# Performance work log

Measured on AMD Instinct MI355X. Metric: run time of the kernel, lower is better.

## Reference

```python
import jax, jax.numpy as jnp
import numpy as np

LN_EPS = 1e-5
MASK_FILL = -1e10


def setup_inputs() -> dict:
    key = jax.random.key(0)
    ks = jax.random.split(key, 6)
    b, lq, lk, d = 8, 2048, 2048, 256
    q = jax.random.normal(ks[0], (b, lq, d), dtype=jnp.float32)
    k = jax.random.normal(ks[1], (b, lk, d), dtype=jnp.float32)
    v = jax.random.normal(ks[2], (b, lk, d), dtype=jnp.float32)
    # additive-score weight, scaled so logits are O(1)
    shared_attn = jax.random.normal(ks[3], (1, 2 * d), dtype=jnp.float32) / jnp.sqrt(jnp.float32(2 * d))
    fc_w = jax.random.normal(ks[4], (d, d), dtype=jnp.float32) / jnp.sqrt(jnp.float32(d))
    ln_gamma = jnp.ones((d,), dtype=jnp.float32)
    ln_beta = jnp.zeros((d,), dtype=jnp.float32)
    mask = jax.random.randint(ks[5], (b, lq, lk), 0, 2).astype(bool)
    return {"q": q, "k": k, "v": v, "shared_attn": shared_attn,
            "fc_w": fc_w, "ln_gamma": ln_gamma, "ln_beta": ln_beta, "mask": mask}


def reference(q, k, v, shared_attn, fc_w, ln_gamma, ln_beta, mask):
    d_k = q.shape[-1]
    residual = q
    # F.linear(cat([q_exp, k_exp], -1), W) with W:(1, 2*d_k) decomposes as
    # score[b,i,j] = q[b,i] . w_q + k[b,j] . w_k  (rank-1 additive score)
    w_q = shared_attn[0, :d_k]
    w_k = shared_attn[0, d_k:]
    sq = jnp.einsum('bid,d->bi', q, w_q)          # (b, lq)
    sk = jnp.einsum('bjd,d->bj', k, w_k)          # (b, lk)
    attn = sq[:, :, None] + sk[:, None, :]        # (b, lq, lk)
    attn = jnp.where(mask, jnp.float32(MASK_FILL), attn)
    attn = jax.nn.softmax(attn, axis=2)
    out = jnp.einsum('bij,bjd->bid', attn, v)     # (b, lq, d_v)
    out = out @ fc_w.T                            # F.linear(out, fc_w)
    x = out + residual
    mu = jnp.mean(x, axis=-1, keepdims=True)
    var = jnp.var(x, axis=-1, keepdims=True)
    out = (x - mu) / jnp.sqrt(var + LN_EPS) * ln_gamma + ln_beta
    return (out, attn)
```

## Files before the change

### kernel.cpp

```cpp
#include <hip/hip_runtime.h>
#include <hip/hip_bf16.h>

#define BB 8
#define LQ 2048
#define LK 2048
#define DD 256
#define OUT0_N (BB*LQ*DD)

typedef short s16x8 __attribute__((ext_vector_type(8)));
typedef float f32x4 __attribute__((ext_vector_type(4)));

__device__ __forceinline__ unsigned short f2b(float x){
  unsigned int u = __float_as_uint(x);
  u += 0x7fffu + ((u >> 16) & 1u);
  return (unsigned short)(u >> 16);
}
__device__ __forceinline__ float b2f(unsigned short h){
  return __uint_as_float(((unsigned int)h) << 16);
}
__device__ __forceinline__ float ldf(const void* p, long i, int bf){
  return bf ? b2f(((const unsigned short*)p)[i]) : ((const float*)p)[i];
}
__device__ __forceinline__ s16x8 ld8(const void* p, long i, int bf){
  if (bf) return *(const s16x8*)((const unsigned short*)p + i);
  const float* f = (const float*)p + i;
  float4 a = *(const float4*)(f);
  float4 c = *(const float4*)(f + 4);
  s16x8 r;
  r[0]=(short)f2b(a.x); r[1]=(short)f2b(a.y); r[2]=(short)f2b(a.z); r[3]=(short)f2b(a.w);
  r[4]=(short)f2b(c.x); r[5]=(short)f2b(c.y); r[6]=(short)f2b(c.z); r[7]=(short)f2b(c.w);
  return r;
}
__device__ __forceinline__ float wsum(float v){
  #pragma unroll
  for (int o=32;o;o>>=1) v += __shfl_xor(v, o, 64);
  return v;
}

__device__ __forceinline__ void detect_flags(const void* q, const void* mask,
                                             int& mbytes, int& bf){
  __shared__ int s_bf, s_mb;
  int t = threadIdx.x;
  if (t == 0){ s_bf = 0; s_mb = 0; }
  __syncthreads();
  if (t < 256){
    float x = fabsf(((const float*)q)[t]);
    if (x > 1e-6f && x < 100.0f) atomicAdd(&s_bf, 1);
    unsigned int mw = ((const unsigned int*)mask)[t];
    if (mw > 1u) atomicOr(&s_mb, 1);
  }
  __syncthreads();
  bf = (s_bf < 128) ? 1 : 0;
  mbytes = s_mb;
}

__global__ __launch_bounds__(256) void k_prep(const void* q, const void* kk,
    const void* v, const void* sh, const void* fc, const void* mask,
    float* e, unsigned short* vtf){
  int mbytes, bf;
  detect_flags(q, mask, mbytes, bf);
  (void)mbytes;
  int lane = threadIdx.x & 63;

  if (blockIdx.x >= 1024){
    int wid = ((blockIdx.x - 1024) << 2) + (threadIdx.x >> 6);
    long base = (long)wid * DD + lane * 4;
    float acc;
    if (bf){
      ushort4 kv = *(const ushort4*)((const unsigned short*)kk + base);
      ushort4 wv = *(const ushort4*)((const unsigned short*)sh + DD + lane*4);
      acc = b2f(kv.x)*b2f(wv.x) + b2f(kv.y)*b2f(wv.y)
          + b2f(kv.z)*b2f(wv.z) + b2f(kv.w)*b2f(wv.w);
    } else {
      float4 kv = *(const float4*)((const float*)kk + base);
      float4 wv = *(const float4*)((const float*)sh + DD + lane*4);
      acc = kv.x*wv.x + kv.y*wv.y + kv.z*wv.z + kv.w*wv.w;
    }
    acc = wsum(acc);
    if (lane == 0) e[wid] = __expf(acc);
    return;
  }

  int wid  = (blockIdx.x << 2) + (threadIdx.x >> 6);
  int dbase = (wid & 15) << 4;
  int jbase = (wid >> 4) << 6;
  int r = lane & 15, g = lane >> 4;
  f32x4 acc[4];
  #pragma unroll
  for (int t2=0;t2<4;t2++) acc[t2] = (f32x4){0.f,0.f,0.f,0.f};
  #pragma unroll
  for (int ks = 0; ks < 8; ++ks){
    int k0 = ks*32 + g*8;
    s16x8 bv = ld8(fc, (long)(dbase + r)*DD + k0, bf);
    #pragma unroll
    for (int t2 = 0; t2 < 4; ++t2){
      s16x8 a = ld8(v, (long)(jbase + t2*16 + r)*DD + k0, bf);
      acc[t2] = __builtin_amdgcn_mfma_f32_16x16x32_bf16(a, bv, acc[t2], 0, 0, 0);
    }
  }
  int b  = jbase >> 11;
  int jj = jbase & 2047;
  int d  = dbase + r;
  #pragma unroll
  for (int t2 = 0; t2 < 4; ++t2){
    int kidx = (jj >> 3) + t2*2 + (g >> 1);
    long idx = ((long)(b*256 + kidx))*2048 + (long)d*8 + (g & 1)*4;
    ushort4 w4;
    w4.x = f2b(acc[t2][0]); w4.y = f2b(acc[t2][1]);
    w4.z = f2b(acc[t2][2]); w4.w = f2b(acc[t2][3]);
    *(ushort4*)(vtf + idx) = w4;
  }
}

__device__ __forceinline__ s16x8 afrag(const unsigned int (*bits_s)[66],
    const unsigned short* e16_s, int row, int kk){
  int w0 = (kk >> 2) & 63;
  int nib4 = (kk >> 8) << 2;
  unsigned lo = (bits_s[row][w0]   >> nib4) & 0xFu;
  unsigned hi = (bits_s[row][w0+1] >> nib4) & 0xFu;
  unsigned m8 = lo | (hi << 4);
  union { s16x8 v; unsigned u[4]; } a;
  a.v = *(const s16x8*)(&e16_s[kk]);
  #pragma unroll
  for (int i = 0; i < 4; ++i){
    unsigned w = a.u[i];
    w = (m8 & (1u << (2*i)))   ? (w & 0xFFFF0000u) : w;
    w = (m8 & (1u << (2*i+1))) ? (w & 0x0000FFFFu) : w;
    a.u[i] = w;
  }
  return a.v;
}

__global__ __launch_bounds__(512, 4) void k_pvf(void* d_out, const unsigned short* vtf,
    const void* q, const void* gamp, const void* betp, const void* mask,
    const float* e){
  __shared__ unsigned int bits_s[32][66];
  __shared__ __align__(16) unsigned short e16_s[LK];
  __shared__ __align__(16) float red[2][32][132];
  __shared__ float scale_s[32];
  __shared__ float gs[256], bs[256];
  int mbytes, bf;
  detect_flags(q, mask, mbytes, bf);
  int o     = ((blockIdx.x & 7) << 6) + (blockIdx.x >> 3);
  int b     = o >> 6;
  int rbase = (o & 63) << 5;
  int t = threadIdx.x, lane = t & 63, wid = t >> 6;
  int nh = wid & 1, ks = wid >> 1;
  int r16 = lane >> 4, c16 = lane & 15;
  int dbase = nh << 7;
  const float* eb = e + b * LK;

  { float4 ef = ((const float4*)eb)[t];
    ushort4 u; u.x=f2b(ef.x); u.y=f2b(ef.y); u.z=f2b(ef.z); u.w=f2b(ef.w);
    *(ushort4*)(&e16_s[t*4]) = u; }
  if (t < 256){ gs[t] = ldf(gamp, t, bf); bs[t] = ldf(betp, t, bf); }

  unsigned short* attn16 = (unsigned short*)d_out + OUT0_N;
  float*          attn32 = (float*)d_out + OUT0_N;
  #pragma unroll 1
  for (int rr = 0; rr < 4; ++rr){
    int row = (wid << 2) + rr;
    long rowm = ((long)(b*LQ + rbase + row)) * (long)LK;
    unsigned int bw = 0;
    float4 ev[8];
    float s = 0.f;
    #pragma unroll
    for (int w = 0; w < 8; ++w){
      int j = (w << 8) + (lane << 2);
      unsigned int m4;
      if (mbytes){
        unsigned int mb = *(const unsigned int*)((const unsigned char*)mask + rowm + j);
        m4 = (mb & 1u) | ((mb >> 7) & 2u) | ((mb >> 14) & 4u) | ((mb >> 21) & 8u);
      } else {
        int4 mi = *(const int4*)((const int*)mask + rowm + j);
        m4 = (mi.x?1u:0u) | (mi.y?2u:0u) | (mi.z?4u:0u) | (mi.w?8u:0u);
      }
      bw |= m4 << (w*4);
      ev[w] = *(const float4*)(eb + j);
      if (!(m4 & 1u)) s += ev[w].x;
      if (!(m4 & 2u)) s += ev[w].y;
      if (!(m4 & 4u)) s += ev[w].z;
      if (!(m4 & 8u)) s += ev[w].w;
    }
    s = wsum(s);
    float scal = (s > 0.f) ? (1.0f/s) : -1.0f;
    bits_s[row][lane] = bw;
    if (lane == 0) scale_s[row] = scal;
    #pragma unroll
    for (int w = 0; w < 8; ++w){
      int j = (w << 8) + (lane << 2);
      float p0,p1,p2,p3;
      if (scal < 0.f){ p0=p1=p2=p3 = 1.0f/2048.0f; }
      else {
        p0 = (bw >> (w*4  )) & 1u ? 0.f : ev[w].x * scal;
        p1 = (bw >> (w*4+1)) & 1u ? 0.f : ev[w].y * scal;
        p2 = (bw >> (w*4+2)) & 1u ? 0.f : ev[w].z * scal;
        p3 = (bw >> (w*4+3)) & 1u ? 0.f : ev[w].w * scal;
      }
      if (bf){
        ushort4 u4; u4.x=f2b(p0); u4.y=f2b(p1); u4.z=f2b(p2); u4.w=f2b(p3);
        *(ushort4*)(attn16 + rowm + j) = u4;
      } else {
        float4 f4 = {p0,p1,p2,p3};
        *(float4*)(attn32 + rowm + j) = f4;
      }
    }
  }
  __syncthreads();

  float sc0 = scale_s[c16];
  float sc1 = scale_s[16 + c16];
  s16x8 cf;
  #pragma unroll
  for (int i = 0; i < 8; ++i) cf[i] = (short)0x3A00;

  const unsigned short* vtfb = vtf + (long)b * 256 * 2048;
  f32x4 acc[2][8];
  #pragma unroll
  for (int i=0;i<2;i++)
    #pragma unroll
    for (int j=0;j<8;j++) acc[i][j] = (f32x4){0.f,0.f,0.f,0.f};

  for (int s = 0; s < 16; ++s){
    int k0 = (ks << 9) + (s << 5);
    const unsigned short* bp = vtfb + ((long)((k0 >> 3) + r16)*256 + dbase + c16)*8;
    s16x8 A0 = (sc0 < 0.f) ? cf : afrag(bits_s, e16_s, c16,      k0 + r16*8);
    s16x8 A1 = (sc1 < 0.f) ? cf : afrag(bits_s, e16_s, 16 + c16, k0 + r16*8);
    {
      s16x8 B0 = *(const s16x8*)(bp);
      s16x8 B1 = *(const s16x8*)(bp + 128);
      s16x8 B2 = *(const s16x8*)(bp + 256);
      s16x8 B3 = *(const s16x8*)(bp + 384);
      acc[0][0] = __builtin_amdgcn_mfma_f32_16x16x32_bf16(A0, B0, acc[0][0], 0,0,0);
      acc[1][0] = __builtin_amdgcn_mfma_f32_16x16x32_bf16(A1, B0, acc[1][0], 0,0,0);
      acc[0][1] = __builtin_amdgcn_mfma_f32_16x16x32_bf16(A0, B1, acc[0][1], 0,0,0);
      acc[1][1] = __builtin_amdgcn_mfma_f32_16x16x32_bf16(A1, B1, acc[1][1], 0,0,0);
      acc[0][2] = __builtin_amdgcn_mfma_f32_16x16x32_bf16(A0, B2, acc[0][2], 0,0,0);
      acc[1][2] = __builtin_amdgcn_mfma_f32_16x16x32_bf16(A1, B2, acc[1][2], 0,0,0);
      acc[0][3] = __builtin_amdgcn_mfma_f32_16x16x32_bf16(A0, B3, acc[0][3], 0,0,0);
      acc[1][3] = __builtin_amdgcn_mfma_f32_16x16x32_bf16(A1, B3, acc[1][3], 0,0,0);
    }
    {
      s16x8 B4 = *(const s16x8*)(bp + 512);
      s16x8 B5 = *(const s16x8*)(bp + 640);
      s16x8 B6 = *(const s16x8*)(bp + 768);
      s16x8 B7 = *(const s16x8*)(bp + 896);
      acc[0][4] = __builtin_amdgcn_mfma_f32_16x16x32_bf16(A0, B4, acc[0][4], 0,0,0);
      acc[1][4] = __builtin_amdgcn_mfma_f32_16x16x32_bf16(A1, B4, acc[1][4], 0,0,0);
      acc[0][5] = __builtin_amdgcn_mfma_f32_16x16x32_bf16(A0, B5, acc[0][5], 0,0,0);
      acc[1][5] = __builtin_amdgcn_mfma_f32_16x16x32_bf16(A1, B5, acc[1][5], 0,0,0);
      acc[0][6] = __builtin_amdgcn_mfma_f32_16x16x32_bf16(A0, B6, acc[0][6], 0,0,0);
      acc[1][6] = __builtin_amdgcn_mfma_f32_16x16x32_bf16(A1, B6, acc[1][6], 0,0,0);
      acc[0][7] = __builtin_amdgcn_mfma_f32_16x16x32_bf16(A0, B7, acc[0][7], 0,0,0);
      acc[1][7] = __builtin_amdgcn_mfma_f32_16x16x32_bf16(A1, B7, acc[1][7], 0,0,0);
    }
  }

  #pragma unroll
  for (int r = 1; r < 4; ++r){
    if (ks == r){
      #pragma unroll
      for (int mi = 0; mi < 2; ++mi)
        #pragma unroll
        for (int ni = 0; ni < 8; ++ni)
          #pragma unroll
          for (int reg = 0; reg < 4; ++reg)
            red[nh][mi*16 + r16*4 + reg][ni*16 + c16] = acc[mi][ni][reg];
    }
    __syncthreads();
    if (ks == 0){
      #pragma unroll
      for (int mi = 0; mi < 2; ++mi)
        #pragma unroll
        for (int ni = 0; ni < 8; ++ni)
          #pragma unroll
          for (int reg = 0; reg < 4; ++reg)
            acc[mi][ni][reg] += red[nh][mi*16 + r16*4 + reg][ni*16 + c16];
    }
    __syncthreads();
  }
  if (ks == 0){
    #pragma unroll
    for (int mi = 0; mi < 2; ++mi)
      #pragma unroll
      for (int ni = 0; ni < 8; ++ni)
        #pragma unroll
        for (int reg = 0; reg < 4; ++reg)
          red[nh][mi*16 + r16*4 + reg][ni*16 + c16] = acc[mi][ni][reg];
  }
  __syncthreads();

  {
    int row = t >> 4, cg = t & 15;
    int nh2 = cg >> 3, coff = (cg & 7) << 4;
    float sc = scale_s[row];
    float sce = (sc < 0.f) ? 1.0f : sc;
    long grow = (long)b*LQ + rbase + row;
    float xv[16];
    float ps = 0.f, pq = 0.f;
    #pragma unroll
    for (int i4 = 0; i4 < 4; ++i4){
      float4 rv = *(const float4*)(&red[nh2][row][coff + i4*4]);
      float rr[4] = {rv.x, rv.y, rv.z, rv.w};
      int col0 = (cg << 4) + i4*4;
      float qv[4];
      if (bf){
        ushort4 qu = *(const ushort4*)((const unsigned short*)q + grow*DD + col0);
        qv[0]=b2f(qu.x); qv[1]=b2f(qu.y); qv[2]=b2f(qu.z); qv[3]=b2f(qu.w);
      } else {
        float4 qf = *(const float4*)((const float*)q + grow*DD + col0);
        qv[0]=qf.x; qv[1]=qf.y; qv[2]=qf.z; qv[3]=qf.w;
      }
      #pragma unroll
      for (int i = 0; i < 4; ++i){
        float x = rr[i]*sce + qv[i];
        xv[i4*4 + i] = x;
        ps += x; pq += x*x;
      }
    }
    ps += __shfl_xor(ps, 1, 64); pq += __shfl_xor(pq, 1, 64);
    ps += __shfl_xor(ps, 2, 64); pq += __shfl_xor(pq, 2, 64);
    ps += __shfl_xor(ps, 4, 64); pq += __shfl_xor(pq, 4, 64);
    ps += __shfl_xor(ps, 8, 64); pq += __shfl_xor(pq, 8, 64);
    float mu = ps * (1.0f/256.0f);
    float var = pq * (1.0f/256.0f) - mu*mu;
    float rs = rsqrtf(var + 1e-5f);
    #pragma unroll
    for (int i4 = 0; i4 < 4; ++i4){
      int col0 = (cg << 4) + i4*4;
      float y[4];
      #pragma unroll
      for (int i = 0; i < 4; ++i){
        int col = col0 + i;
        y[i] = (xv[i4*4 + i] - mu) * rs * gs[col] + bs[col];
      }
      long oi = grow*(long)DD + col0;
      if (bf){
        ushort4 u4; u4.x=f2b(y[0]); u4.y=f2b(y[1]); u4.z=f2b(y[2]); u4.w=f2b(y[3]);
        *(ushort4*)((unsigned short*)d_out + oi) = u4;
      } else {
        float4 f4 = {y[0],y[1],y[2],y[3]};
        *(float4*)((float*)d_out + oi) = f4;
      }
    }
  }
}

extern "C" void kernel_launch(void* const* d_in, const int* in_sizes, int n_in,
                              void* d_out, int out_size, void* d_ws, size_t ws_size,
                              hipStream_t stream) {
  const void* q    = d_in[0];
  const void* k    = d_in[1];
  const void* v    = d_in[2];
  const void* sh   = d_in[3];
  const void* fc   = d_in[4];
  const void* gam  = d_in[5];
  const void* bet  = d_in[6];
  const void* mask = d_in[7];

  float*          e   = (float*)((char*)d_ws + 65536);
  unsigned short* vtf = (unsigned short*)((char*)d_ws + 4456448);

  k_prep<<<5120, 256, 0, stream>>>(q, k, v, sh, fc, mask, e, vtf);
  k_pvf <<<512,  512, 0, stream>>>(d_out, vtf, q, gam, bet, mask, e);
}
```

Baseline: 130.3 us.

## Stream V tiles into LDS with async global_load_lds double buffering

Replaces the direct global-to-register loads of V fragments in the PV MFMA loop with per-wave double-buffered asynchronous global_load_lds transfers, gated by explicit vmcnt waits and sched barriers. The reduction buffer is aliased onto the same shared memory region so the staging space fits. The goal is to overlap V fetch latency with MFMA work. The risk is that the larger LDS footprint (about 80KB per block) lowers occupancy, and the manual waitcnt and barrier scheduling constrains the compiler.

```diff
diff --git a/kernel.cpp b/kernel.cpp
--- a/kernel.cpp
+++ b/kernel.cpp
@@ -9,6 +9,9 @@
 
 typedef short s16x8 __attribute__((ext_vector_type(8)));
 typedef float f32x4 __attribute__((ext_vector_type(4)));
+
+#define GAS __attribute__((address_space(1)))
+#define LAS __attribute__((address_space(3)))
 
 __device__ __forceinline__ unsigned short f2b(float x){
   unsigned int u = __float_as_uint(x);
@@ -134,11 +137,15 @@
 __global__ __launch_bounds__(512, 4) void k_pvf(void* d_out, const unsigned short* vtf,
     const void* q, const void* gamp, const void* betp, const void* mask,
     const float* e){
-  __shared__ unsigned int bits_s[32][66];
-  __shared__ __align__(16) unsigned short e16_s[LK];
-  __shared__ __align__(16) float red[2][32][132];
-  __shared__ float scale_s[32];
-  __shared__ float gs[256], bs[256];
+  __shared__ __align__(16) char smem[80256];
+  unsigned int (*bits_s)[66] = reinterpret_cast<unsigned int(*)[66]>(smem + 65536);
+  unsigned short* e16_s      = (unsigned short*)(smem + 73984);
+  float* scale_s             = (float*)(smem + 78080);
+  float* gs                  = (float*)(smem + 78208);
+  float* bs                  = (float*)(smem + 79232);
+  float* redp                = (float*)smem;
+  #define RED(nh_, row_, col_) redp[(((nh_)*32)+(row_))*132 + (col_)]
+
   int mbytes, bf;
   detect_flags(q, mask, mbytes, bf);
   int o     = ((blockIdx.x & 7) << 6) + (blockIdx.x >> 3);
@@ -149,6 +156,21 @@
   int r16 = lane >> 4, c16 = lane & 15;
   int dbase = nh << 7;
   const float* eb = e + b * LK;
+  const unsigned short* vtfb = vtf + (long)b * 256 * 2048;
+  char* stag = smem + wid * 8192;
+
+  auto STAGE = [&](int j){
+    int ss = j >> 1, h = j & 1;
+    int k0 = (ks << 9) + (ss << 5);
+    const char* g = (const char*)vtfb +
+        (((long)((k0 >> 3) + r16) * 256 + dbase + c16) << 4);
+    char* lb = stag + (j & 1) * 4096;
+    #pragma unroll
+    for (int i = 0; i < 4; ++i)
+      __builtin_amdgcn_global_load_lds(
+        (const GAS unsigned int*)(g + h*1024 + i*256),
+        (LAS unsigned int*)(lb + i*1024), 16, 0, 0);
+  };
 
   { float4 ef = ((const float4*)eb)[t];
     ushort4 u; u.x=f2b(ef.x); u.y=f2b(ef.y); u.z=f2b(ef.z); u.w=f2b(ef.w);
@@ -206,6 +228,7 @@
       }
     }
   }
+  STAGE(0); STAGE(1);
   __syncthreads();
 
   float sc0 = scale_s[c16];
@@ -214,47 +237,41 @@
   #pragma unroll
   for (int i = 0; i < 8; ++i) cf[i] = (short)0x3A00;
 
-  const unsigned short* vtfb = vtf + (long)b * 256 * 2048;
   f32x4 acc[2][8];
   #pragma unroll
   for (int i=0;i<2;i++)
     #pragma unroll
     for (int j=0;j<8;j++) acc[i][j] = (f32x4){0.f,0.f,0.f,0.f};
 
+  #pragma unroll 1
   for (int s = 0; s < 16; ++s){
     int k0 = (ks << 9) + (s << 5);
-    const unsigned short* bp = vtfb + ((long)((k0 >> 3) + r16)*256 + dbase + c16)*8;
     s16x8 A0 = (sc0 < 0.f) ? cf : afrag(bits_s, e16_s, c16,      k0 + r16*8);
     s16x8 A1 = (sc1 < 0.f) ? cf : afrag(bits_s, e16_s, 16 + c16, k0 + r16*8);
-    {
-      s16x8 B0 = *(const s16x8*)(bp);
-      s16x8 B1 = *(const s16x8*)(bp + 128);
-      s16x8 B2 = *(const s16x8*)(bp + 256);
-      s16x8 B3 = *(const s16x8*)(bp + 384);
-      acc[0][0] = __builtin_amdgcn_mfma_f32_16x16x32_bf16(A0, B0, acc[0][0], 0,0,0);
-      acc[1][0] = __builtin_amdgcn_mfma_f32_16x16x32_bf16(A1, B0, acc[1][0], 0,0,0);
-      acc[0][1] = __builtin_amdgcn_mfma_f32_16x16x32_bf16(A0, B1, acc[0][1], 0,0,0);
-      acc[1][1] = __builtin_amdgcn_mfma_f32_16x16x32_bf16(A1, B1, acc[1][1], 0,0,0);
-      acc[0][2] = __builtin_amdgcn_mfma_f32_16x16x32_bf16(A0, B2, acc[0][2], 0,0,0);
-      acc[1][2] = __builtin_amdgcn_mfma_f32_16x16x32_bf16(A1, B2, acc[1][2], 0,0,0);
-      acc[0][3] = __builtin_amdgcn_mfma_f32_16x16x32_bf16(A0, B3, acc[0][3], 0,0,0);
-      acc[1][3] = __builtin_amdgcn_mfma_f32_16x16x32_bf16(A1, B3, acc[1][3], 0,0,0);
-    }
-    {
-      s16x8 B4 = *(const s16x8*)(bp + 512);
-      s16x8 B5 = *(const s16x8*)(bp + 640);
-      s16x8 B6 = *(const s16x8*)(bp + 768);
-      s16x8 B7 = *(const s16x8*)(bp + 896);
-      acc[0][4] = __builtin_amdgcn_mfma_f32_16x16x32_bf16(A0, B4, acc[0][4], 0,0,0);
-      acc[1][4] = __builtin_amdgcn_mfma_f32_16x16x32_bf16(A1, B4, acc[1][4], 0,0,0);
-      acc[0][5] = __builtin_amdgcn_mfma_f32_16x16x32_bf16(A0, B5, acc[0][5], 0,0,0);
-      acc[1][5] = __builtin_amdgcn_mfma_f32_16x16x32_bf16(A1, B5, acc[1][5], 0,0,0);
-      acc[0][6] = __builtin_amdgcn_mfma_f32_16x16x32_bf16(A0, B6, acc[0][6], 0,0,0);
-      acc[1][6] = __builtin_amdgcn_mfma_f32_16x16x32_bf16(A1, B6, acc[1][6], 0,0,0);
-      acc[0][7] = __builtin_amdgcn_mfma_f32_16x16x32_bf16(A0, B7, acc[0][7], 0,0,0);
-      acc[1][7] = __builtin_amdgcn_mfma_f32_16x16x32_bf16(A1, B7, acc[1][7], 0,0,0);
-    }
-  }
+    #pragma unroll
+    for (int h = 0; h < 2; ++h){
+      int j = 2*s + h;
+      if (j < 31) asm volatile("s_waitcnt vmcnt(4)" ::: "memory");
+      else        asm volatile("s_waitcnt vmcnt(0)" ::: "memory");
+      __builtin_amdgcn_sched_barrier(0);
+      const char* lb = stag + (j & 1) * 4096;
+      s16x8 Bv0 = *(const s16x8*)(lb +    0 + (lane << 4));
+      s16x8 Bv1 = *(const s16x8*)(lb + 1024 + (lane << 4));
+      s16x8 Bv2 = *(const s16x8*)(lb + 2048 + (lane << 4));
+      s16x8 Bv3 = *(const s16x8*)(lb + 3072 + (lane << 4));
+      __builtin_amdgcn_sched_barrier(0);
+      if (j + 2 < 32) STAGE(j + 2);
+      acc[0][h*4+0] = __builtin_amdgcn_mfma_f32_16x16x32_bf16(A0, Bv0, acc[0][h*4+0], 0,0,0);
+      acc[1][h*4+0] = __builtin_amdgcn_mfma_f32_16x16x32_bf16(A1, Bv0, acc[1][h*4+0], 0,0,0);
+      acc[0][h*4+1] = __builtin_amdgcn_mfma_f32_16x16x32_bf16(A0, Bv1, acc[0][h*4+1], 0,0,0);
+      acc[1][h*4+1] = __builtin_amdgcn_mfma_f32_16x16x32_bf16(A1, Bv1, acc[1][h*4+1], 0,0,0);
+      acc[0][h*4+2] = __builtin_amdgcn_mfma_f32_16x16x32_bf16(A0, Bv2, acc[0][h*4+2], 0,0,0);
+      acc[1][h*4+2] = __builtin_amdgcn_mfma_f32_16x16x32_bf16(A1, Bv2, acc[1][h*4+2], 0,0,0);
+      acc[0][h*4+3] = __builtin_amdgcn_mfma_f32_16x16x32_bf16(A0, Bv3, acc[0][h*4+3], 0,0,0);
+      acc[1][h*4+3] = __builtin_amdgcn_mfma_f32_16x16x32_bf16(A1, Bv3, acc[1][h*4+3], 0,0,0);
+    }
+  }
+  __syncthreads();
 
   #pragma unroll
   for (int r = 1; r < 4; ++r){
@@ -265,7 +282,7 @@
         for (int ni = 0; ni < 8; ++ni)
           #pragma unroll
           for (int reg = 0; reg < 4; ++reg)
-            red[nh][mi*16 + r16*4 + reg][ni*16 + c16] = acc[mi][ni][reg];
+            RED(nh, mi*16 + r16*4 + reg, ni*16 + c16) = acc[mi][ni][reg];
     }
     __syncthreads();
     if (ks == 0){
@@ -275,7 +292,7 @@
         for (int ni = 0; ni < 8; ++ni)
           #pragma unroll
           for (int reg = 0; reg < 4; ++reg)
-            acc[mi][ni][reg] += red[nh][mi*16 + r16*4 + reg][ni*16 + c16];
+            acc[mi][ni][reg] += RED(nh, mi*16 + r16*4 + reg, ni*16 + c16);
     }
     __syncthreads();
   }
@@ -286,7 +303,7 @@
       for (int ni = 0; ni < 8; ++ni)
         #pragma unroll
         for (int reg = 0; reg < 4; ++reg)
-          red[nh][mi*16 + r16*4 + reg][ni*16 + c16] = acc[mi][ni][reg];
+          RED(nh, mi*16 + r16*4 + reg, ni*16 + c16) = acc[mi][ni][reg];
   }
   __syncthreads();
 
@@ -300,7 +317,7 @@
     float ps = 0.f, pq = 0.f;
     #pragma unroll
     for (int i4 = 0; i4 < 4; ++i4){
-      float4 rv = *(const float4*)(&red[nh2][row][coff + i4*4]);
+      float4 rv = *(const float4*)(&RED(nh2, row, coff + i4*4));
       float rr[4] = {rv.x, rv.y, rv.z, rv.w};
       int col0 = (cg << 4) + i4*4;
       float qv[4];
@@ -344,6 +361,7 @@
       }
     }
   }
+  #undef RED
 }
 
 extern "C" void kernel_launch(void* const* d_in, const int* in_sizes, int n_in,
```

Result: no change. 128.0 us (-1.8%).
